# Optimization experiments

Measured on AMD Instinct MI355X. Metric: run time of the kernel, lower is better.

## Reference

```python
import jax, jax.numpy as jnp
import numpy as np

HIDDEN = 1024
HEADS = 16
BATCH = 2
SEQ = 2048
# dropout_p = 0.1 but module evaluated in eval mode (training=False) -> identity


def setup_inputs() -> dict:
    key = jax.random.key(0)
    k1, k2, k3 = jax.random.split(key, 3)
    x = jax.random.normal(k1, (BATCH, SEQ, HIDDEN), dtype=jnp.float32)
    # unit-scaling Linear: weight ~ N(0,1) (reset_parameters uses nn.init.normal_)
    w_qkv = jax.random.normal(k2, (3 * HIDDEN, HIDDEN), dtype=jnp.float32)
    w_o = jax.random.normal(k3, (HIDDEN, HIDDEN), dtype=jnp.float32)
    return {"x": x, "w_qkv": w_qkv, "w_o": w_o}


def reference(x, w_qkv, w_o):
    b, s, hid = x.shape
    heads = HEADS
    d = hid // heads
    # unit-scaled linear (constraint='to_output_scale'): y = x @ W.T * fan_in**-0.5
    qkv = (x @ w_qkv.T) * (hid ** -0.5)            # [b, s, 3*hid]
    # einops 'b s (z h d) -> z b h s d'
    qkv = qkv.reshape(b, s, 3, heads, d)
    q = jnp.transpose(qkv[:, :, 0], (0, 2, 1, 3))   # [b, h, s, d]
    k = jnp.transpose(qkv[:, :, 1], (0, 2, 1, 3))
    v = jnp.transpose(qkv[:, :, 2], (0, 2, 1, 3))
    # unit-scaled matmul: scale = inner_dim**-0.5
    scores = jnp.einsum('bhqd,bhkd->bhqk', q, k) * (d ** -0.5)  # [b, h, s, s]
    # unit-scaled softmax: output_scale = n / sqrt(n - 1)
    attn = jax.nn.softmax(scores, axis=-1) * (s / np.sqrt(s - 1.0))
    # dropout inactive (eval mode)
    out = jnp.einsum('bhqk,bhkd->bhqd', attn, v) * (s ** -0.5)  # inner dim = s
    out = jnp.transpose(out, (0, 2, 1, 3)).reshape(b, s, hid)   # 'b h s d -> b s (h d)'
    return (out @ w_o.T) * (hid ** -0.5)
```

## Files before the change

kernel.cpp:

```cpp
#include <hip/hip_runtime.h>

typedef unsigned short u16;
typedef _Float16 f16x8 __attribute__((ext_vector_type(8)));
typedef _Float16 f16x4 __attribute__((ext_vector_type(4)));
typedef _Float16 f16x2 __attribute__((ext_vector_type(2)));
typedef float f32x4 __attribute__((ext_vector_type(4)));
typedef unsigned short u16x4 __attribute__((ext_vector_type(4)));

#define HID 1024
#define SEQ 2048
#define NH 16
#define DH 64

__device__ __forceinline__ u16 f2h(float f) {
  return __builtin_bit_cast(u16, (_Float16)f);
}
__device__ __forceinline__ f32x4 mfma_h(f16x8 a, f16x8 b, f32x4 c) {
  return __builtin_amdgcn_mfma_f32_16x16x32_f16(a, b, c, 0, 0, 0);
}
__device__ __forceinline__ float fexp2(float x) {
#if __has_builtin(__builtin_amdgcn_exp2f)
  return __builtin_amdgcn_exp2f(x);
#else
  return __expf(0.69314718f * x);
#endif
}
__device__ __forceinline__ f16x2 pkrtz(float a, float b) {
  return __builtin_bit_cast(f16x2, __builtin_amdgcn_cvt_pkrtz(a, b));
}
__device__ __forceinline__ void g2l16(const u16* g, u16* l) {
  __builtin_amdgcn_global_load_lds(
      (const __attribute__((address_space(1))) unsigned int*)g,
      (__attribute__((address_space(3))) unsigned int*)l, 16, 0, 0);
}

#define NX4 ((4096 * 1024) / 4)
#define NQ4 ((3072 * 1024) / 4)
#define NO4 ((1024 * 1024) / 4)
__global__ __launch_bounds__(256) void prep_kernel(
    const float* __restrict__ x, const float* __restrict__ wq,
    const float* __restrict__ wo,
    u16* __restrict__ x16, u16* __restrict__ wq16, u16* __restrict__ wo16) {
  int i = blockIdx.x * 256 + threadIdx.x;
  const float4 v = (i < NX4) ? ((const float4*)x)[i]
                 : (i < NX4 + NQ4) ? ((const float4*)wq)[i - NX4]
                 : ((const float4*)wo)[i - NX4 - NQ4];
  u16* dst = (i < NX4) ? &x16[(size_t)i * 4]
           : (i < NX4 + NQ4) ? &wq16[(size_t)(i - NX4) * 4]
           : &wo16[(size_t)(i - NX4 - NQ4) * 4];
  u16x4 o;
  o[0] = f2h(v.x); o[1] = f2h(v.y); o[2] = f2h(v.z); o[3] = f2h(v.w);
  *(u16x4*)dst = o;
}

__global__ __launch_bounds__(256, 3) void gemm_qkv(
    const u16* __restrict__ a16, const u16* __restrict__ b16,
    u16* __restrict__ qf, u16* __restrict__ kf, u16* __restrict__ vtf) {
  __shared__ __align__(16) u16 la[2][128 * 32], lb[2][128 * 32];
  const int t = threadIdx.x;
  const int lane = t & 63, w = t >> 6;
  const int wr = w >> 1, wc = w & 1;
  const int lr = lane & 15, lg = lane >> 4;
  const int br = blockIdx.x, bc = blockIdx.y;
  const f32x4 fzero = {0.f, 0.f, 0.f, 0.f};
  f32x4 acc[4][4];
#pragma unroll
  for (int i = 0; i < 4; ++i)
#pragma unroll
    for (int j = 0; j < 4; ++j) acc[i][j] = fzero;
  const int srow = t >> 2;
  const int scol = ((t & 3) ^ ((srow + (srow >> 2)) & 3)) << 3;
  const u16* ga = a16 + (size_t)(br * 128 + srow) * HID + scol;
  const u16* gb = b16 + (size_t)(bc * 128 + srow) * HID + scol;
  const int lo16 = t * 8;

#define QSTAGE(buf, s)                                        \
  {                                                           \
    const int kk = (s) * 32;                                  \
    g2l16(ga + kk, &la[buf][lo16]);                           \
    g2l16(ga + kk + (size_t)64 * HID, &la[buf][lo16 + 2048]); \
    g2l16(gb + kk, &lb[buf][lo16]);                           \
    g2l16(gb + kk + (size_t)64 * HID, &lb[buf][lo16 + 2048]); \
  }

  QSTAGE(0, 0)
  for (int s = 0; s < 32; ++s) {
    const int cur = s & 1;
    __syncthreads();
    if (s + 1 < 32) QSTAGE(cur ^ 1, s + 1)
    f16x8 ah[4], bh[4];
#pragma unroll
    for (int i = 0; i < 4; ++i) {
      int row = wr * 64 + i * 16 + lr;
      ah[i] = *(const f16x8*)&la[cur][row * 32 + ((lg ^ ((row + (row >> 2)) & 3)) << 3)];
    }
#pragma unroll
    for (int j = 0; j < 4; ++j) {
      int row = wc * 64 + j * 16 + lr;
      bh[j] = *(const f16x8*)&lb[cur][row * 32 + ((lg ^ ((row + (row >> 2)) & 3)) << 3)];
    }
#pragma unroll
    for (int i = 0; i < 4; ++i)
#pragma unroll
      for (int j = 0; j < 4; ++j) acc[i][j] = mfma_h(ah[i], bh[j], acc[i][j]);
  }
#undef QSTAGE

  const int m0 = br * 128 + wr * 64;
  const int b = m0 >> 11, sbase = m0 & 2047;
  const int hcol = bc * 2 + wc;
  const int z = hcol >> 4, hh = hcol & 15;
  const int bhid = b * NH + hh;
  if (z == 2) {
#pragma unroll
    for (int i = 0; i < 4; ++i) {
      int s2b = sbase + ((i >> 1) << 5) + (lg << 3) + ((i & 1) << 2);
#pragma unroll
      for (int j = 0; j < 4; ++j) {
        int d = j * 16 + lr;
        u16x4 o;
#pragma unroll
        for (int r = 0; r < 4; ++r) o[r] = f2h(acc[i][j][r] * 0.03125f);
        *(u16x4*)&vtf[((size_t)bhid * DH + d) * SEQ + s2b] = o;
      }
    }
  } else {
    const float sc = (z == 0) ? 0.03125f * 0.18033688f : 0.03125f;
    u16* dst = (z == 0) ? qf : kf;
#pragma unroll
    for (int i = 0; i < 4; ++i)
#pragma unroll
      for (int j = 0; j < 4; ++j) {
        int d = j * 16 + lr;
#pragma unroll
        for (int r = 0; r < 4; ++r) {
          int ss = sbase + i * 16 + lg * 4 + r;
          dst[((size_t)bhid * SEQ + ss) * DH + d] = f2h(acc[i][j][r] * sc);
        }
      }
  }
}

__global__ __launch_bounds__(256, 2) void gemm_proj(
    const u16* __restrict__ po0, const u16* __restrict__ po1,
    const float* __restrict__ pl, const u16* __restrict__ b16,
    float* __restrict__ out) {
  __shared__ __align__(16) u16 la[2][128 * 64];
  __shared__ __align__(16) u16 lb[2][64 * 64];
  __shared__ float linv[16 * 128];
  const int t = threadIdx.x;
  const int lane = t & 63, w = t >> 6;
  const int wr = w >> 1, wc = w & 1;
  const int lr = lane & 15, lg = lane >> 4;
  const int br = blockIdx.x, bc = blockIdx.y;
  const f32x4 fzero = {0.f, 0.f, 0.f, 0.f};
  f32x4 acc[4][2];
#pragma unroll
  for (int i = 0; i < 4; ++i)
#pragma unroll
    for (int j = 0; j < 2; ++j) acc[i][j] = fzero;
#pragma unroll
  for (int jj = 0; jj < 8; ++jj) {
    int idx = t + jj * 256;
    int h = idx >> 7, i = idx & 127;
    int ar = br * 128 + i;
    int b = ar >> 11, s = ar & 2047;
    int bhs = (b * NH + h) * SEQ + s;
    linv[idx] = 1.00024426f / (pl[bhs] + pl[NH * 2 * SEQ + bhs]);
  }
  const int srow = t >> 3, scol = ((t & 7) ^ (srow & 7)) << 3;
  const u16* gp0 = po0 + (size_t)(br * 128 + srow) * HID + scol;
  const u16* gp1 = po1 + (size_t)(br * 128 + srow) * HID + scol;
  const u16* gb = b16 + (size_t)(bc * 64 + srow) * HID + scol;
  const int lo16 = t * 8;
  f16x8 a0[4], a1[4];

#define PLOADA(s)                                                   \
  {                                                                 \
    const int kk = (s) * 64;                                        \
    _Pragma("unroll") for (int r = 0; r < 4; ++r) {                 \
      a0[r] = *(const f16x8*)(gp0 + kk + (size_t)(r * 32) * HID);   \
      a1[r] = *(const f16x8*)(gp1 + kk + (size_t)(r * 32) * HID);   \
    }                                                               \
  }
#define PSTAGEB(buf, s)                                             \
  {                                                                 \
    const int kk = (s) * 64;                                        \
    g2l16(gb + kk, &lb[buf][lo16]);                                 \
    g2l16(gb + kk + (size_t)32 * HID, &lb[buf][lo16 + 2048]);       \
  }
#define PCOMBINE(buf, s)                                            \
  {                                                                 \
    _Pragma("unroll") for (int r = 0; r < 4; ++r) {                 \
      float invr = linv[((s) << 7) + srow + r * 32];                \
      union { f16x2 h2[4]; f16x8 h8; } uo;                          \
      _Pragma("unroll") for (int p = 0; p < 4; ++p) {               \
        float s0 = ((float)a0[r][2 * p] + (float)a1[r][2 * p]) * invr;        \
        float s1 = ((float)a0[r][2 * p + 1] + (float)a1[r][2 * p + 1]) * invr;\
        uo.h2[p] = pkrtz(s0, s1);                                   \
      }                                                             \
      *(f16x8*)&la[buf][lo16 + r * 2048] = uo.h8;                   \
    }                                                               \
  }

  __syncthreads();
  PLOADA(0)
  PSTAGEB(0, 0)
  PCOMBINE(0, 0)

  for (int s = 0; s < 16; ++s) {
    const int cur = s & 1;
    __syncthreads();
    if (s + 1 < 16) {
      PLOADA(s + 1)
      PSTAGEB(cur ^ 1, s + 1)
    }
#pragma unroll
    for (int ks = 0; ks < 2; ++ks) {
      f16x8 ah[4], bh[2];
#pragma unroll
      for (int i = 0; i < 4; ++i) {
        int row = wr * 64 + i * 16 + lr;
        ah[i] = *(const f16x8*)&la[cur][row * 64 + (((ks * 4 + lg) ^ (row & 7)) << 3)];
      }
#pragma unroll
      for (int j = 0; j < 2; ++j) {
        int row = wc * 32 + j * 16 + lr;
        bh[j] = *(const f16x8*)&lb[cur][row * 64 + (((ks * 4 + lg) ^ (row & 7)) << 3)];
      }
#pragma unroll
      for (int i = 0; i < 4; ++i)
#pragma unroll
        for (int j = 0; j < 2; ++j)
          acc[i][j] = mfma_h(ah[i], bh[j], acc[i][j]);
    }
    if (s + 1 < 16) PCOMBINE(cur ^ 1, s + 1)
  }
#undef PLOADA
#undef PSTAGEB
#undef PCOMBINE

  const int m0 = br * 128 + wr * 64, n0 = bc * 64 + wc * 32;
#pragma unroll
  for (int i = 0; i < 4; ++i)
#pragma unroll
    for (int j = 0; j < 2; ++j)
#pragma unroll
      for (int r = 0; r < 4; ++r) {
        int row = m0 + i * 16 + lg * 4 + r;
        int col = n0 + j * 16 + lr;
        out[(size_t)row * HID + col] = acc[i][j][r] * 0.03125f;
      }
}

__global__ __launch_bounds__(256, 4) void attn_kernel(
    const u16* __restrict__ qf, const u16* __restrict__ kf,
    const u16* __restrict__ vtf, u16* __restrict__ po0,
    u16* __restrict__ po1, float* __restrict__ pl) {
  __shared__ __align__(16) u16 lk[2][64 * 64];
  __shared__ __align__(16) u16 lv[2][64 * 64];
  const int t = threadIdx.x;
  const int lane = t & 63, w = t >> 6;
  const int lr = lane & 15, lg = lane >> 4;
  const int bh = blockIdx.x, qt = blockIdx.y, sp = blockIdx.z;
  const size_t base_qk = (size_t)bh * SEQ * DH;
  const size_t base_vt = (size_t)bh * DH * SEQ;

  f16x8 qfr[2][2];
#pragma unroll
  for (int rt = 0; rt < 2; ++rt)
#pragma unroll
    for (int ks = 0; ks < 2; ++ks)
      qfr[rt][ks] = *(const f16x8*)&qf[base_qk +
          (size_t)(qt * 128 + w * 32 + rt * 16 + lr) * DH + ks * 32 + lg * 8];

  f16x8 vones;
#pragma unroll
  for (int j = 0; j < 8; ++j) vones[j] = (_Float16)1.0f;

  const f32x4 fzero = {0.f, 0.f, 0.f, 0.f};
  f32x4 acc_o[2][4];
  f32x4 acc_l[2];
#pragma unroll
  for (int rt = 0; rt < 2; ++rt) {
    acc_l[rt] = fzero;
#pragma unroll
    for (int ct = 0; ct < 4; ++ct) acc_o[rt][ct] = fzero;
  }

  const int srow = t >> 3;
  const int scol = ((t & 7) ^ (srow & 7)) << 3;
  const int lo16 = t * 8;

  const u16* gk0 = kf + base_qk + (size_t)(sp * 1024 + srow) * DH + scol;
  const u16* gv0 = vtf + base_vt + (size_t)srow * SEQ + sp * 1024 + scol;

#define STAGE(buf, j)                                             \
  {                                                               \
    const u16* gk = gk0 + (size_t)(j) * 64 * DH;                  \
    g2l16(gk, &lk[buf][lo16]);                                    \
    g2l16(gk + 32 * DH, &lk[buf][lo16 + 2048]);                   \
    const u16* gv = gv0 + (j) * 64;                               \
    g2l16(gv, &lv[buf][lo16]);                                    \
    g2l16(gv + (size_t)32 * SEQ, &lv[buf][lo16 + 2048]);          \
  }

  STAGE(0, 0)

  for (int j = 0; j < 16; ++j) {
    const int cur = j & 1;
    __syncthreads();

    f32x4 sa[2][4];
    __builtin_amdgcn_s_setprio(1);
#pragma unroll
    for (int ct = 0; ct < 4; ++ct) {
      int row = ct * 16 + lr;
      f16x8 k0 = *(const f16x8*)&lk[cur][row * 64 + ((lg ^ (row & 7)) << 3)];
      f16x8 k1 = *(const f16x8*)&lk[cur][row * 64 + (((4 + lg) ^ (row & 7)) << 3)];
      sa[0][ct] = mfma_h(k0, qfr[0][0], fzero);
      sa[1][ct] = mfma_h(k0, qfr[1][0], fzero);
      sa[0][ct] = mfma_h(k1, qfr[0][1], sa[0][ct]);
      sa[1][ct] = mfma_h(k1, qfr[1][1], sa[1][ct]);
    }
    __builtin_amdgcn_s_setprio(0);

    if (j + 1 < 16) STAGE(cur ^ 1, j + 1)

    f16x8 pfr[2][2];
#pragma unroll
    for (int rt = 0; rt < 2; ++rt)
#pragma unroll
      for (int ks = 0; ks < 2; ++ks) {
        union { f16x2 h2[4]; f16x8 h8; } up;
#pragma unroll
        for (int hi = 0; hi < 2; ++hi) {
          float e0 = fexp2(sa[rt][ks * 2 + hi][0]);
          float e1 = fexp2(sa[rt][ks * 2 + hi][1]);
          float e2 = fexp2(sa[rt][ks * 2 + hi][2]);
          float e3 = fexp2(sa[rt][ks * 2 + hi][3]);
          up.h2[hi * 2] = pkrtz(e0, e1);
          up.h2[hi * 2 + 1] = pkrtz(e2, e3);
        }
        pfr[rt][ks] = up.h8;
      }

    __builtin_amdgcn_s_setprio(1);
#pragma unroll
    for (int ks = 0; ks < 2; ++ks)
#pragma unroll
      for (int ct = 0; ct < 4; ++ct) {
        int vrow = ct * 16 + lr;
        f16x8 vfr = *(const f16x8*)&lv[cur][vrow * 64 + (((ks * 4 + lg) ^ (vrow & 7)) << 3)];
#pragma unroll
        for (int rt = 0; rt < 2; ++rt) acc_o[rt][ct] = mfma_h(pfr[rt][ks], vfr, acc_o[rt][ct]);
      }
#pragma unroll
    for (int rt = 0; rt < 2; ++rt) {
      acc_l[rt] = mfma_h(pfr[rt][0], vones, acc_l[rt]);
      acc_l[rt] = mfma_h(pfr[rt][1], vones, acc_l[rt]);
    }
    __builtin_amdgcn_s_setprio(0);
  }

  const int b = bh >> 4, hh = bh & 15;
  u16* pob = sp ? po1 : po0;
  float* plb = pl + sp * (NH * 2 * SEQ);
#pragma unroll
  for (int rt = 0; rt < 2; ++rt)
#pragma unroll
    for (int r = 0; r < 4; ++r) {
      int s = qt * 128 + w * 32 + rt * 16 + lg * 4 + r;
      int row = b * SEQ + s;
      if (lr == 0) plb[bh * SEQ + s] = acc_l[rt][r];
#pragma unroll
      for (int ct = 0; ct < 4; ++ct) {
        int d = ct * 16 + lr;
        pob[(size_t)row * HID + hh * DH + d] = f2h(acc_o[rt][ct][r]);
      }
    }
}

extern "C" void kernel_launch(void* const* d_in, const int* in_sizes, int n_in,
                              void* d_out, int out_size, void* d_ws, size_t ws_size,
                              hipStream_t stream) {
  const float* x = (const float*)d_in[0];
  const float* w_qkv = (const float*)d_in[1];
  const float* w_o = (const float*)d_in[2];
  u16* ws = (u16*)d_ws;
  const size_t XS = (size_t)4096 * 1024;
  const size_t WQ = (size_t)3072 * 1024;
  const size_t WO = (size_t)1024 * 1024;
  u16* x16  = ws;           u16* wq16 = x16 + XS;
  u16* wo16 = wq16 + WQ;
  u16* q_f  = wo16 + WO;    u16* k_f  = q_f + XS;
  u16* vt_f = k_f + XS;     u16* po0  = vt_f + XS;
  u16* po1  = x16;
  float* pl = (float*)wq16;

  prep_kernel<<<(NX4 + NQ4 + NO4) / 256, 256, 0, stream>>>(
      x, w_qkv, w_o, x16, wq16, wo16);
  gemm_qkv<<<dim3(32, 24), 256, 0, stream>>>(x16, wq16, q_f, k_f, vt_f);
  attn_kernel<<<dim3(32, 16, 2), 256, 0, stream>>>(q_f, k_f, vt_f, po0, po1, pl);
  gemm_proj<<<dim3(32, 16), 256, 0, stream>>>(po0, po1, pl, wo16, (float*)d_out);
}
```

Baseline: 179.9 us.

## Load QKV GEMM fragments directly from global memory, dropping LDS staging

The QKV projection GEMM no longer stages A and B tiles through double-buffered shared memory with barriers. Each wave now loads its MFMA fragments straight from global memory into registers, using register double-buffering so the next k-slice loads while the current one computes. This removes LDS traffic and __syncthreads. In exchange, waves in the same block fetch overlapping rows redundantly, relying on L1/L2 to absorb it, and register pressure goes up.

Measured after the change: 236.4 us. 31.4% more time.

```diff
diff --git a/kernel.cpp b/kernel.cpp
--- a/kernel.cpp
+++ b/kernel.cpp
@@ -56,7 +56,6 @@
 __global__ __launch_bounds__(256, 3) void gemm_qkv(
     const u16* __restrict__ a16, const u16* __restrict__ b16,
     u16* __restrict__ qf, u16* __restrict__ kf, u16* __restrict__ vtf) {
-  __shared__ __align__(16) u16 la[2][128 * 32], lb[2][128 * 32];
   const int t = threadIdx.x;
   const int lane = t & 63, w = t >> 6;
   const int wr = w >> 1, wc = w & 1;
@@ -68,43 +67,40 @@
   for (int i = 0; i < 4; ++i)
 #pragma unroll
     for (int j = 0; j < 4; ++j) acc[i][j] = fzero;
-  const int srow = t >> 2;
-  const int scol = ((t & 3) ^ ((srow + (srow >> 2)) & 3)) << 3;
-  const u16* ga = a16 + (size_t)(br * 128 + srow) * HID + scol;
-  const u16* gb = b16 + (size_t)(bc * 128 + srow) * HID + scol;
-  const int lo16 = t * 8;
-
-#define QSTAGE(buf, s)                                        \
-  {                                                           \
-    const int kk = (s) * 32;                                  \
-    g2l16(ga + kk, &la[buf][lo16]);                           \
-    g2l16(ga + kk + (size_t)64 * HID, &la[buf][lo16 + 2048]); \
-    g2l16(gb + kk, &lb[buf][lo16]);                           \
-    g2l16(gb + kk + (size_t)64 * HID, &lb[buf][lo16 + 2048]); \
-  }
-
-  QSTAGE(0, 0)
-  for (int s = 0; s < 32; ++s) {
-    const int cur = s & 1;
-    __syncthreads();
-    if (s + 1 < 32) QSTAGE(cur ^ 1, s + 1)
-    f16x8 ah[4], bh[4];
-#pragma unroll
-    for (int i = 0; i < 4; ++i) {
-      int row = wr * 64 + i * 16 + lr;
-      ah[i] = *(const f16x8*)&la[cur][row * 32 + ((lg ^ ((row + (row >> 2)) & 3)) << 3)];
-    }
-#pragma unroll
-    for (int j = 0; j < 4; ++j) {
-      int row = wc * 64 + j * 16 + lr;
-      bh[j] = *(const f16x8*)&lb[cur][row * 32 + ((lg ^ ((row + (row >> 2)) & 3)) << 3)];
-    }
-#pragma unroll
-    for (int i = 0; i < 4; ++i)
-#pragma unroll
-      for (int j = 0; j < 4; ++j) acc[i][j] = mfma_h(ah[i], bh[j], acc[i][j]);
-  }
-#undef QSTAGE
+
+  const u16* pa[4];
+  const u16* pb[4];
+#pragma unroll
+  for (int i = 0; i < 4; ++i)
+    pa[i] = a16 + (size_t)(br * 128 + wr * 64 + i * 16 + lr) * HID + lg * 8;
+#pragma unroll
+  for (int j = 0; j < 4; ++j)
+    pb[j] = b16 + (size_t)(bc * 128 + wc * 64 + j * 16 + lr) * HID + lg * 8;
+
+  f16x8 fa0[4], fb0[4], fa1[4], fb1[4];
+#define LDF(FA, FB, kk)                                   \
+  {                                                       \
+    _Pragma("unroll") for (int i = 0; i < 4; ++i)         \
+        FA[i] = *(const f16x8*)(pa[i] + (kk));            \
+    _Pragma("unroll") for (int j = 0; j < 4; ++j)         \
+        FB[j] = *(const f16x8*)(pb[j] + (kk));            \
+  }
+#define FMA16(FA, FB)                                     \
+  {                                                       \
+    _Pragma("unroll") for (int i = 0; i < 4; ++i)         \
+        _Pragma("unroll") for (int j = 0; j < 4; ++j)     \
+            acc[i][j] = mfma_h(FA[i], FB[j], acc[i][j]);  \
+  }
+
+  LDF(fa0, fb0, 0)
+  for (int kk = 0; kk < HID; kk += 64) {
+    LDF(fa1, fb1, kk + 32)
+    FMA16(fa0, fb0)
+    if (kk + 64 < HID) LDF(fa0, fb0, kk + 64)
+    FMA16(fa1, fb1)
+  }
+#undef LDF
+#undef FMA16
 
   const int m0 = br * 128 + wr * 64;
   const int b = m0 >> 11, sbase = m0 & 2047;
```
